# Performance work log

Measured on AMD Instinct MI355X. Metric: run time of the kernel, lower is better.

## Reference

```python
import jax, jax.numpy as jnp
import numpy as np

N = 8192      # total factor-graph rows (detection nodes + association nodes)
ND = N // 2   # detection-node rows; rest are association (edge) rows
D_RAW = 74    # raw input dim; last 10 cols = convex hull (5 points x 2 coords)
EPS = 1e-5    # BatchNorm eps


def _adjs():
    # signed factor-graph adjacencies with self-loops marking row type
    rng = np.random.RandomState(0)
    deg = 8
    node_adj = np.zeros((N, N), np.float32)
    edge_adj = np.zeros((N, N), np.float32)
    nbr = rng.randint(ND, N, size=(ND, deg))
    node_adj[np.repeat(np.arange(ND), deg), nbr.ravel()] = rng.choice([-1.0, 1.0], ND * deg).astype(np.float32)
    node_adj[np.arange(ND), np.arange(ND)] = 1.0
    nbr2 = rng.randint(0, ND, size=(N - ND, deg))
    edge_adj[np.repeat(np.arange(ND, N), deg), nbr2.ravel()] = rng.choice([-1.0, 1.0], (N - ND) * deg).astype(np.float32)
    edge_adj[np.arange(ND, N), np.arange(ND, N)] = 1.0
    return jnp.asarray(node_adj), jnp.asarray(edge_adj)


def setup_inputs() -> dict:
    key = jax.random.key(0)
    ks = jax.random.split(key, 16)
    node_adj, edge_adj = _adjs()

    def lin(k, fi, fo):
        return jax.random.normal(k, (fi, fo), jnp.float32) / np.sqrt(fi)

    inp = {"x": jax.random.normal(ks[0], (N, D_RAW), jnp.float32),
           "node_adj": node_adj, "edge_adj": edge_adj}
    # PointNetfeatsmall: 1x1 conv stack 3->16->32->64 with eval-mode BatchNorm
    for i, (fi, fo) in enumerate([(3, 16), (16, 32), (32, 64)], 1):
        k = jax.random.split(ks[i], 5)
        inp[f"pn_w{i}"] = lin(k[0], fi, fo)
        inp[f"pn_b{i}"] = 0.1 * jax.random.normal(k[1], (fo,), jnp.float32)
        inp[f"pn_g{i}"] = 1.0 + 0.1 * jax.random.normal(k[2], (fo,), jnp.float32)
        inp[f"pn_be{i}"] = 0.1 * jax.random.normal(k[3], (fo,), jnp.float32)
        inp[f"pn_m{i}"] = 0.1 * jax.random.normal(k[4], (fo,), jnp.float32)
        inp[f"pn_v{i}"] = jnp.ones((fo,), jnp.float32)
    # FactorGraphConvolution weights (msg_type='concat' -> in dim doubles)
    for i, (fi, fo) in enumerate([(256, 64), (128, 64), (128, 1)], 1):
        k = jax.random.split(ks[10 + i], 2)
        inp[f"gc{i}_wn"] = lin(k[0], fi, fo)
        inp[f"gc{i}_we"] = lin(k[1], fi, fo)
        inp[f"gc{i}_bn"] = jnp.zeros((fo,), jnp.float32)
        inp[f"gc{i}_be"] = jnp.zeros((fo,), jnp.float32)
    inp["gc3_bn"] = jnp.full((1,), -4.595, jnp.float32)  # nn.init.constant_ in TrackMPNN.__init__
    inp["gc3_be"] = jnp.full((1,), 4.595, jnp.float32)
    return inp


def _bn(h, g, b, m, v):  # h: [N, C, P], eval-mode BatchNorm1d
    return (h - m[:, None]) * (g[:, None] / jnp.sqrt(v[:, None] + EPS)) + b[:, None]


def _fgc(h, node_adj, edge_adj, wn, we, bn_, be_, relu):
    # concat(self, aggregated-neighbors) -> linear; node/edge rows use their own branch
    node_out = jnp.concatenate([h, node_adj @ h], axis=1) @ wn + bn_
    edge_out = jnp.concatenate([h, edge_adj @ h], axis=1) @ we + be_
    out = jnp.where((jnp.diag(node_adj) != 0)[:, None], node_out, edge_out)
    return jax.nn.relu(out) if relu else out


def reference(x, node_adj, edge_adj,
              pn_w1, pn_b1, pn_g1, pn_be1, pn_m1, pn_v1,
              pn_w2, pn_b2, pn_g2, pn_be2, pn_m2, pn_v2,
              pn_w3, pn_b3, pn_g3, pn_be3, pn_m3, pn_v3,
              gc1_wn, gc1_we, gc1_bn, gc1_be,
              gc2_wn, gc2_we, gc2_bn, gc2_be,
              gc3_wn, gc3_we, gc3_bn, gc3_be):
    # convex hull branch: [N, 3, 5] (third coordinate zero-padded)
    ch = jnp.concatenate([x[:, -10:].reshape(-1, 2, 5),
                          jnp.zeros((x.shape[0], 1, 5), x.dtype)], axis=1)
    h = jax.nn.relu(_bn(jnp.einsum('ncp,cd->ndp', ch, pn_w1) + pn_b1[:, None], pn_g1, pn_be1, pn_m1, pn_v1))
    h = jax.nn.relu(_bn(jnp.einsum('ncp,cd->ndp', h, pn_w2) + pn_b2[:, None], pn_g2, pn_be2, pn_m2, pn_v2))
    h = _bn(jnp.einsum('ncp,cd->ndp', h, pn_w3) + pn_b3[:, None], pn_g3, pn_be3, pn_m3, pn_v3)
    feat = h.max(axis=2)                       # PointNet global max pool -> [N, 64]
    h = jnp.concatenate([x[:, :-10], feat], axis=1)  # [N, 128]
    h = _fgc(h, node_adj, edge_adj, gc1_wn, gc1_we, gc1_bn, gc1_be, True)
    h = _fgc(h, node_adj, edge_adj, gc2_wn, gc2_we, gc2_bn, gc2_be, True)
    h = _fgc(h, node_adj, edge_adj, gc3_wn, gc3_we, gc3_bn, gc3_be, False)
    return jax.nn.sigmoid(h)                   # [N, 1]
```

## Files before the change

kernel.cpp:

```cpp
#include <hip/hip_runtime.h>
#include <math.h>

#define NROWS 8192
#define NDET  4096

static constexpr int OFF_SGN = 65536;
static constexpr int OFF_PN  = 131072;
static constexpr int OFF_H1  = 1703936;
static constexpr int OFF_H2  = 2228224;

__global__ __launch_bounds__(256) void k_front(
    const float* __restrict__ nodeA, const float* __restrict__ edgeA,
    int* __restrict__ idx, float* __restrict__ sgn,
    const float* __restrict__ x,
    const float* __restrict__ w1, const float* __restrict__ b1,
    const float* __restrict__ g1, const float* __restrict__ be1,
    const float* __restrict__ m1, const float* __restrict__ v1,
    const float* __restrict__ w2, const float* __restrict__ b2,
    const float* __restrict__ g2, const float* __restrict__ be2,
    const float* __restrict__ m2, const float* __restrict__ v2,
    const float* __restrict__ w3, const float* __restrict__ b3,
    const float* __restrict__ g3, const float* __restrict__ be3,
    const float* __restrict__ m3, const float* __restrict__ v3,
    float* __restrict__ pn)
{
    __shared__ int   scnt;
    __shared__ float fw[2720];
    int t = threadIdx.x;

    if (blockIdx.x >= 512) {
        int row = blockIdx.x - 512;
        const float* src; int col0;
        if (row < NDET) { src = nodeA + (size_t)row * NROWS + NDET; col0 = NDET; }
        else            { src = edgeA + (size_t)row * NROWS;        col0 = 0;    }
        if (t == 0) scnt = 0;
        __syncthreads();
        const float4* s4 = (const float4*)src;
        #pragma unroll
        for (int it = 0; it < 4; ++it) {
            float4 v = s4[t + it * 256];
            int cb = col0 + (t + it * 256) * 4;
            if (v.x != 0.f) { int p = atomicAdd(&scnt, 1); idx[row * 8 + p] = cb;     sgn[row * 8 + p] = v.x; }
            if (v.y != 0.f) { int p = atomicAdd(&scnt, 1); idx[row * 8 + p] = cb + 1; sgn[row * 8 + p] = v.y; }
            if (v.z != 0.f) { int p = atomicAdd(&scnt, 1); idx[row * 8 + p] = cb + 2; sgn[row * 8 + p] = v.z; }
            if (v.w != 0.f) { int p = atomicAdd(&scnt, 1); idx[row * 8 + p] = cb + 3; sgn[row * 8 + p] = v.w; }
        }
        __syncthreads();
        for (int p = scnt + t; p < 8; p += 256) { idx[row * 8 + p] = 0; sgn[row * 8 + p] = 0.f; }
        return;
    }

    for (int i = t; i < 48; i += 256)  { int d = i & 15; fw[i]       = w1[i] * g1[d] * rsqrtf(v1[d] + 1e-5f); }
    for (int i = t; i < 16; i += 256)  {                 fw[48 + i]  = (b1[i] - m1[i]) * g1[i] * rsqrtf(v1[i] + 1e-5f) + be1[i]; }
    for (int i = t; i < 512; i += 256) { int d = i & 31; fw[64 + i]  = w2[i] * g2[d] * rsqrtf(v2[d] + 1e-5f); }
    for (int i = t; i < 32; i += 256)  {                 fw[576 + i] = (b2[i] - m2[i]) * g2[i] * rsqrtf(v2[i] + 1e-5f) + be2[i]; }
    for (int i = t; i < 2048; i += 256){ int d = i & 63; fw[608 + i] = w3[i] * g3[d] * rsqrtf(v3[d] + 1e-5f); }
    for (int i = t; i < 64; i += 256)  {                 fw[2656 + i]= (b3[i] - m3[i]) * g3[i] * rsqrtf(v3[i] + 1e-5f) + be3[i]; }
    __syncthreads();

    int lane = t & 63;
    int wv   = t >> 6;
    int l15  = lane & 15, l31 = lane & 31;
    int rowbase = (blockIdx.x * 4 + wv) * 4;

    for (int r = rowbase; r < rowbase + 4; ++r) {
        float val  = (lane < 10) ? x[(size_t)r * 74 + 64 + lane] : 0.f;
        float vmax = -3.0e38f;
        #pragma unroll
        for (int p = 0; p < 5; ++p) {
            float a0 = __shfl(val, p, 64);
            float a1 = __shfl(val, p + 5, 64);
            float h1v = fmaxf(0.f, a0 * fw[l15] + a1 * fw[16 + l15] + fw[48 + l15]);
            float s2 = fw[576 + l31];
            #pragma unroll
            for (int d = 0; d < 16; ++d)
                s2 += __shfl(h1v, d, 64) * fw[64 + d * 32 + l31];
            float h2v = fmaxf(0.f, s2);
            float s3 = fw[2656 + lane];
            #pragma unroll
            for (int e = 0; e < 32; ++e)
                s3 += __shfl(h2v, e, 64) * fw[608 + e * 64 + lane];
            vmax = fmaxf(vmax, s3);
        }
        pn[(size_t)r * 64 + lane] = vmax;
    }
}

__global__ __launch_bounds__(256) void k_fgc1(
    const float* __restrict__ x, const float* __restrict__ pn,
    const int* __restrict__ idx, const float* __restrict__ sgn,
    const float* __restrict__ wn, const float* __restrict__ we,
    const float* __restrict__ bn, const float* __restrict__ be,
    float* __restrict__ out)
{
    __shared__ float inb[16 * 260];
    __shared__ int   lidx[128];
    __shared__ float lsgn[128];
    int t = threadIdx.x;
    int r0 = blockIdx.x * 16;
    if (t < 128) {
        int ir = t >> 3, j = t & 7;
        lidx[t] = idx[(r0 + ir) * 8 + j];
        lsgn[t] = sgn[(r0 + ir) * 8 + j];
    }
    __syncthreads();

    int f   = t & 127;
    int rrb = t >> 7;
    #pragma unroll
    for (int pass = 0; pass < 8; ++pass) {
        int rr = rrb + pass * 2;
        int r  = r0 + rr;
        float own = (f < 64) ? x[(size_t)r * 74 + f] : pn[(size_t)r * 64 + (f - 64)];
        float acc = own;
        #pragma unroll
        for (int j = 0; j < 8; ++j) {
            int nb   = lidx[rr * 8 + j];
            float sg = lsgn[rr * 8 + j];
            float v  = (f < 64) ? x[(size_t)nb * 74 + f] : pn[(size_t)nb * 64 + (f - 64)];
            acc += sg * v;
        }
        inb[rr * 260 + f]       = own;
        inb[rr * 260 + 128 + f] = acc;
    }
    __syncthreads();

    int r_l = t >> 4, cg = t & 15, c0 = cg * 4;
    bool isnode = (blockIdx.x < 256);
    const float* W = isnode ? wn : we;
    const float* B = isnode ? bn : be;
    float a0 = B[c0], a1 = B[c0 + 1], a2 = B[c0 + 2], a3 = B[c0 + 3];
    #pragma unroll
    for (int kg = 0; kg < 64; ++kg) {
        float4 a = *(const float4*)&inb[r_l * 260 + kg * 4];
        const float* av = &a.x;
        #pragma unroll
        for (int kk = 0; kk < 4; ++kk) {
            float4 w = *(const float4*)&W[(kg * 4 + kk) * 64 + c0];
            a0 += av[kk] * w.x; a1 += av[kk] * w.y;
            a2 += av[kk] * w.z; a3 += av[kk] * w.w;
        }
    }
    float4 o;
    o.x = fmaxf(a0, 0.f); o.y = fmaxf(a1, 0.f);
    o.z = fmaxf(a2, 0.f); o.w = fmaxf(a3, 0.f);
    *(float4*)&out[(size_t)(r0 + r_l) * 64 + c0] = o;
}

__global__ __launch_bounds__(256) void k_fgc2(
    const float* __restrict__ h, const int* __restrict__ idx,
    const float* __restrict__ sgn,
    const float* __restrict__ wn, const float* __restrict__ we,
    const float* __restrict__ bn, const float* __restrict__ be,
    float* __restrict__ out)
{
    __shared__ float inb[16 * 132];
    __shared__ int   lidx[128];
    __shared__ float lsgn[128];
    int t = threadIdx.x;
    int r0 = blockIdx.x * 16;
    if (t < 128) {
        int ir = t >> 3, j = t & 7;
        lidx[t] = idx[(r0 + ir) * 8 + j];
        lsgn[t] = sgn[(r0 + ir) * 8 + j];
    }
    __syncthreads();

    int f   = t & 63;
    int rrb = t >> 6;
    #pragma unroll
    for (int pass = 0; pass < 4; ++pass) {
        int rr = rrb + pass * 4;
        int r  = r0 + rr;
        float own = h[(size_t)r * 64 + f];
        float acc = own;
        #pragma unroll
        for (int j = 0; j < 8; ++j) {
            int nb   = lidx[rr * 8 + j];
            float sg = lsgn[rr * 8 + j];
            acc += sg * h[(size_t)nb * 64 + f];
        }
        inb[rr * 132 + f]      = own;
        inb[rr * 132 + 64 + f] = acc;
    }
    __syncthreads();

    int r_l = t >> 4, cg = t & 15, c0 = cg * 4;
    bool isnode = (blockIdx.x < 256);
    const float* W = isnode ? wn : we;
    const float* B = isnode ? bn : be;
    float a0 = B[c0], a1 = B[c0 + 1], a2 = B[c0 + 2], a3 = B[c0 + 3];
    #pragma unroll
    for (int kg = 0; kg < 32; ++kg) {
        float4 a = *(const float4*)&inb[r_l * 132 + kg * 4];
        const float* av = &a.x;
        #pragma unroll
        for (int kk = 0; kk < 4; ++kk) {
            float4 w = *(const float4*)&W[(kg * 4 + kk) * 64 + c0];
            a0 += av[kk] * w.x; a1 += av[kk] * w.y;
            a2 += av[kk] * w.z; a3 += av[kk] * w.w;
        }
    }
    float4 o;
    o.x = fmaxf(a0, 0.f); o.y = fmaxf(a1, 0.f);
    o.z = fmaxf(a2, 0.f); o.w = fmaxf(a3, 0.f);
    *(float4*)&out[(size_t)(r0 + r_l) * 64 + c0] = o;
}

__global__ __launch_bounds__(256) void k_gc3(
    const float* __restrict__ h2, const int* __restrict__ idx,
    const float* __restrict__ sgn,
    const float* __restrict__ wn, const float* __restrict__ we,
    const float* __restrict__ bn, const float* __restrict__ be,
    float* __restrict__ out)
{
    int lane = threadIdx.x & 63;
    int row  = blockIdx.x * 4 + (threadIdx.x >> 6);
    float own = h2[(size_t)row * 64 + lane];
    float agg = own;
    #pragma unroll
    for (int j = 0; j < 8; ++j) {
        int nb   = idx[row * 8 + j];
        float sg = sgn[row * 8 + j];
        agg += sg * h2[(size_t)nb * 64 + lane];
    }
    bool isnode = row < NDET;
    const float* w = isnode ? wn : we;
    float bias = isnode ? bn[0] : be[0];
    float acc = own * w[lane] + agg * w[64 + lane];
    #pragma unroll
    for (int off = 32; off > 0; off >>= 1)
        acc += __shfl_xor(acc, off, 64);
    if (lane == 0)
        out[row] = 1.f / (1.f + expf(-(acc + bias)));
}

extern "C" void kernel_launch(void* const* d_in, const int* in_sizes, int n_in,
                              void* d_out, int out_size, void* d_ws, size_t ws_size,
                              hipStream_t stream)
{
    const float* x     = (const float*)d_in[0];
    const float* nodeA = (const float*)d_in[1];
    const float* edgeA = (const float*)d_in[2];
    const float* pw1 = (const float*)d_in[3];  const float* pb1 = (const float*)d_in[4];
    const float* pg1 = (const float*)d_in[5];  const float* pe1 = (const float*)d_in[6];
    const float* pm1 = (const float*)d_in[7];  const float* pv1 = (const float*)d_in[8];
    const float* pw2 = (const float*)d_in[9];  const float* pb2 = (const float*)d_in[10];
    const float* pg2 = (const float*)d_in[11]; const float* pe2 = (const float*)d_in[12];
    const float* pm2 = (const float*)d_in[13]; const float* pv2 = (const float*)d_in[14];
    const float* pw3 = (const float*)d_in[15]; const float* pb3 = (const float*)d_in[16];
    const float* pg3 = (const float*)d_in[17]; const float* pe3 = (const float*)d_in[18];
    const float* pm3 = (const float*)d_in[19]; const float* pv3 = (const float*)d_in[20];
    const float* g1wn = (const float*)d_in[21]; const float* g1we = (const float*)d_in[22];
    const float* g1bn = (const float*)d_in[23]; const float* g1be = (const float*)d_in[24];
    const float* g2wn = (const float*)d_in[25]; const float* g2we = (const float*)d_in[26];
    const float* g2bn = (const float*)d_in[27]; const float* g2be = (const float*)d_in[28];
    const float* g3wn = (const float*)d_in[29]; const float* g3we = (const float*)d_in[30];
    const float* g3bn = (const float*)d_in[31]; const float* g3be = (const float*)d_in[32];

    float* ws  = (float*)d_ws;
    int*   idx = (int*)ws;
    float* sgn = ws + OFF_SGN;
    float* pn  = ws + OFF_PN;
    float* h1  = ws + OFF_H1;
    float* h2  = ws + OFF_H2;
    float* out = (float*)d_out;

    k_front<<<512 + NROWS, 256, 0, stream>>>(nodeA, edgeA, idx, sgn, x,
        pw1, pb1, pg1, pe1, pm1, pv1,
        pw2, pb2, pg2, pe2, pm2, pv2,
        pw3, pb3, pg3, pe3, pm3, pv3, pn);
    k_fgc1<<<512, 256, 0, stream>>>(x, pn, idx, sgn, g1wn, g1we, g1bn, g1be, h1);
    k_fgc2<<<512, 256, 0, stream>>>(h1, idx, sgn, g2wn, g2we, g2bn, g2be, h2);
    k_gc3<<<2048, 256, 0, stream>>>(h2, idx, sgn, g3wn, g3we, g3bn, g3be, out);
}
```

Before: 522.8 us.

## Fuse three graph-conv layers into one persistent kernel with grid barriers

Merges the three graph-convolution kernels into a single 512-block kernel separated by software grid-wide barriers built on atomic counters, which k_front resets each call. This removes two kernel launches and their gaps, and lets each block keep its neighbour index and sign lists in shared memory across layers. In exchange it depends on all 512 blocks being co-resident to avoid deadlock, and adds spin-wait barrier cost.

```diff
diff --git a/kernel.cpp b/kernel.cpp
--- a/kernel.cpp
+++ b/kernel.cpp
@@ -8,6 +8,9 @@
 static constexpr int OFF_PN  = 131072;
 static constexpr int OFF_H1  = 1703936;
 static constexpr int OFF_H2  = 2228224;
+static constexpr int OFF_BAR = 2752512;
+
+#define TAIL_BLOCKS 512
 
 __global__ __launch_bounds__(256) void k_front(
     const float* __restrict__ nodeA, const float* __restrict__ edgeA,
@@ -22,7 +25,7 @@
     const float* __restrict__ w3, const float* __restrict__ b3,
     const float* __restrict__ g3, const float* __restrict__ be3,
     const float* __restrict__ m3, const float* __restrict__ v3,
-    float* __restrict__ pn)
+    float* __restrict__ pn, int* __restrict__ bar)
 {
     __shared__ int   scnt;
     __shared__ float fw[2720];
@@ -50,6 +53,8 @@
         return;
     }
 
+    if (blockIdx.x == 0 && t < 2) bar[t] = 0;
+
     for (int i = t; i < 48; i += 256)  { int d = i & 15; fw[i]       = w1[i] * g1[d] * rsqrtf(v1[d] + 1e-5f); }
     for (int i = t; i < 16; i += 256)  {                 fw[48 + i]  = (b1[i] - m1[i]) * g1[i] * rsqrtf(v1[i] + 1e-5f) + be1[i]; }
     for (int i = t; i < 512; i += 256) { int d = i & 31; fw[64 + i]  = w2[i] * g2[d] * rsqrtf(v2[d] + 1e-5f); }
@@ -86,18 +91,38 @@
     }
 }
 
-__global__ __launch_bounds__(256) void k_fgc1(
+__device__ __forceinline__ void gridbar(int* cnt)
+{
+    __syncthreads();
+    if (threadIdx.x == 0) {
+        __threadfence();
+        __hip_atomic_fetch_add(cnt, 1, __ATOMIC_RELEASE, __HIP_MEMORY_SCOPE_AGENT);
+        while (__hip_atomic_load(cnt, __ATOMIC_ACQUIRE, __HIP_MEMORY_SCOPE_AGENT) < TAIL_BLOCKS)
+            __builtin_amdgcn_s_sleep(2);
+    }
+    __syncthreads();
+    __threadfence();
+}
+
+__global__ __launch_bounds__(256, 2) void k_tail(
     const float* __restrict__ x, const float* __restrict__ pn,
     const int* __restrict__ idx, const float* __restrict__ sgn,
-    const float* __restrict__ wn, const float* __restrict__ we,
-    const float* __restrict__ bn, const float* __restrict__ be,
-    float* __restrict__ out)
+    const float* __restrict__ g1wn, const float* __restrict__ g1we,
+    const float* __restrict__ g1bn, const float* __restrict__ g1be,
+    const float* __restrict__ g2wn, const float* __restrict__ g2we,
+    const float* __restrict__ g2bn, const float* __restrict__ g2be,
+    const float* __restrict__ g3wn, const float* __restrict__ g3we,
+    const float* __restrict__ g3bn, const float* __restrict__ g3be,
+    float* __restrict__ h1, float* __restrict__ h2, float* __restrict__ out,
+    int* bar)
 {
     __shared__ float inb[16 * 260];
     __shared__ int   lidx[128];
     __shared__ float lsgn[128];
     int t = threadIdx.x;
     int r0 = blockIdx.x * 16;
+    bool isnode = (blockIdx.x < 256);
+
     if (t < 128) {
         int ir = t >> 3, j = t & 7;
         lidx[t] = idx[(r0 + ir) * 8 + j];
@@ -105,134 +130,110 @@
     }
     __syncthreads();
 
-    int f   = t & 127;
-    int rrb = t >> 7;
-    #pragma unroll
-    for (int pass = 0; pass < 8; ++pass) {
-        int rr = rrb + pass * 2;
-        int r  = r0 + rr;
-        float own = (f < 64) ? x[(size_t)r * 74 + f] : pn[(size_t)r * 64 + (f - 64)];
-        float acc = own;
-        #pragma unroll
-        for (int j = 0; j < 8; ++j) {
-            int nb   = lidx[rr * 8 + j];
-            float sg = lsgn[rr * 8 + j];
-            float v  = (f < 64) ? x[(size_t)nb * 74 + f] : pn[(size_t)nb * 64 + (f - 64)];
-            acc += sg * v;
-        }
-        inb[rr * 260 + f]       = own;
-        inb[rr * 260 + 128 + f] = acc;
-    }
-    __syncthreads();
-
-    int r_l = t >> 4, cg = t & 15, c0 = cg * 4;
-    bool isnode = (blockIdx.x < 256);
-    const float* W = isnode ? wn : we;
-    const float* B = isnode ? bn : be;
-    float a0 = B[c0], a1 = B[c0 + 1], a2 = B[c0 + 2], a3 = B[c0 + 3];
-    #pragma unroll
-    for (int kg = 0; kg < 64; ++kg) {
-        float4 a = *(const float4*)&inb[r_l * 260 + kg * 4];
-        const float* av = &a.x;
-        #pragma unroll
-        for (int kk = 0; kk < 4; ++kk) {
-            float4 w = *(const float4*)&W[(kg * 4 + kk) * 64 + c0];
-            a0 += av[kk] * w.x; a1 += av[kk] * w.y;
-            a2 += av[kk] * w.z; a3 += av[kk] * w.w;
-        }
-    }
-    float4 o;
-    o.x = fmaxf(a0, 0.f); o.y = fmaxf(a1, 0.f);
-    o.z = fmaxf(a2, 0.f); o.w = fmaxf(a3, 0.f);
-    *(float4*)&out[(size_t)(r0 + r_l) * 64 + c0] = o;
-}
-
-__global__ __launch_bounds__(256) void k_fgc2(
-    const float* __restrict__ h, const int* __restrict__ idx,
-    const float* __restrict__ sgn,
-    const float* __restrict__ wn, const float* __restrict__ we,
-    const float* __restrict__ bn, const float* __restrict__ be,
-    float* __restrict__ out)
-{
-    __shared__ float inb[16 * 132];
-    __shared__ int   lidx[128];
-    __shared__ float lsgn[128];
-    int t = threadIdx.x;
-    int r0 = blockIdx.x * 16;
-    if (t < 128) {
-        int ir = t >> 3, j = t & 7;
-        lidx[t] = idx[(r0 + ir) * 8 + j];
-        lsgn[t] = sgn[(r0 + ir) * 8 + j];
-    }
-    __syncthreads();
-
-    int f   = t & 63;
-    int rrb = t >> 6;
-    #pragma unroll
-    for (int pass = 0; pass < 4; ++pass) {
-        int rr = rrb + pass * 4;
-        int r  = r0 + rr;
-        float own = h[(size_t)r * 64 + f];
-        float acc = own;
-        #pragma unroll
-        for (int j = 0; j < 8; ++j) {
-            int nb   = lidx[rr * 8 + j];
-            float sg = lsgn[rr * 8 + j];
-            acc += sg * h[(size_t)nb * 64 + f];
-        }
-        inb[rr * 132 + f]      = own;
-        inb[rr * 132 + 64 + f] = acc;
-    }
-    __syncthreads();
-
-    int r_l = t >> 4, cg = t & 15, c0 = cg * 4;
-    bool isnode = (blockIdx.x < 256);
-    const float* W = isnode ? wn : we;
-    const float* B = isnode ? bn : be;
-    float a0 = B[c0], a1 = B[c0 + 1], a2 = B[c0 + 2], a3 = B[c0 + 3];
-    #pragma unroll
-    for (int kg = 0; kg < 32; ++kg) {
-        float4 a = *(const float4*)&inb[r_l * 132 + kg * 4];
-        const float* av = &a.x;
-        #pragma unroll
-        for (int kk = 0; kk < 4; ++kk) {
-            float4 w = *(const float4*)&W[(kg * 4 + kk) * 64 + c0];
-            a0 += av[kk] * w.x; a1 += av[kk] * w.y;
-            a2 += av[kk] * w.z; a3 += av[kk] * w.w;
-        }
-    }
-    float4 o;
-    o.x = fmaxf(a0, 0.f); o.y = fmaxf(a1, 0.f);
-    o.z = fmaxf(a2, 0.f); o.w = fmaxf(a3, 0.f);
-    *(float4*)&out[(size_t)(r0 + r_l) * 64 + c0] = o;
-}
-
-__global__ __launch_bounds__(256) void k_gc3(
-    const float* __restrict__ h2, const int* __restrict__ idx,
-    const float* __restrict__ sgn,
-    const float* __restrict__ wn, const float* __restrict__ we,
-    const float* __restrict__ bn, const float* __restrict__ be,
-    float* __restrict__ out)
-{
-    int lane = threadIdx.x & 63;
-    int row  = blockIdx.x * 4 + (threadIdx.x >> 6);
-    float own = h2[(size_t)row * 64 + lane];
-    float agg = own;
-    #pragma unroll
-    for (int j = 0; j < 8; ++j) {
-        int nb   = idx[row * 8 + j];
-        float sg = sgn[row * 8 + j];
-        agg += sg * h2[(size_t)nb * 64 + lane];
-    }
-    bool isnode = row < NDET;
-    const float* w = isnode ? wn : we;
-    float bias = isnode ? bn[0] : be[0];
-    float acc = own * w[lane] + agg * w[64 + lane];
-    #pragma unroll
-    for (int off = 32; off > 0; off >>= 1)
-        acc += __shfl_xor(acc, off, 64);
-    if (lane == 0)
-        out[row] = 1.f / (1.f + expf(-(acc + bias)));
+    {
+        int f = t & 127, rrb = t >> 7;
+        #pragma unroll
+        for (int pass = 0; pass < 8; ++pass) {
+            int rr = rrb + pass * 2;
+            int r  = r0 + rr;
+            float own = (f < 64) ? x[(size_t)r * 74 + f] : pn[(size_t)r * 64 + (f - 64)];
+            float acc = own;
+            #pragma unroll
+            for (int j = 0; j < 8; ++j) {
+                int nb   = lidx[rr * 8 + j];
+                float sg = lsgn[rr * 8 + j];
+                float v  = (f < 64) ? x[(size_t)nb * 74 + f] : pn[(size_t)nb * 64 + (f - 64)];
+                acc += sg * v;
+            }
+            inb[rr * 260 + f]       = own;
+            inb[rr * 260 + 128 + f] = acc;
+        }
+        __syncthreads();
+        int r_l = t >> 4, c0 = (t & 15) * 4;
+        const float* W = isnode ? g1wn : g1we;
+        const float* B = isnode ? g1bn : g1be;
+        float a0 = B[c0], a1 = B[c0 + 1], a2 = B[c0 + 2], a3 = B[c0 + 3];
+        #pragma unroll
+        for (int kg = 0; kg < 64; ++kg) {
+            float4 a = *(const float4*)&inb[r_l * 260 + kg * 4];
+            const float* av = &a.x;
+            #pragma unroll
+            for (int kk = 0; kk < 4; ++kk) {
+                float4 w = *(const float4*)&W[(kg * 4 + kk) * 64 + c0];
+                a0 += av[kk] * w.x; a1 += av[kk] * w.y;
+                a2 += av[kk] * w.z; a3 += av[kk] * w.w;
+            }
+        }
+        float4 o;
+        o.x = fmaxf(a0, 0.f); o.y = fmaxf(a1, 0.f);
+        o.z = fmaxf(a2, 0.f); o.w = fmaxf(a3, 0.f);
+        *(float4*)&h1[(size_t)(r0 + r_l) * 64 + c0] = o;
+    }
+    gridbar(&bar[0]);
+    __syncthreads();
+
+    {
+        int f = t & 63, rrb = t >> 6;
+        #pragma unroll
+        for (int pass = 0; pass < 4; ++pass) {
+            int rr = rrb + pass * 4;
+            int r  = r0 + rr;
+            float own = h1[(size_t)r * 64 + f];
+            float acc = own;
+            #pragma unroll
+            for (int j = 0; j < 8; ++j) {
+                int nb   = lidx[rr * 8 + j];
+                float sg = lsgn[rr * 8 + j];
+                acc += sg * h1[(size_t)nb * 64 + f];
+            }
+            inb[rr * 132 + f]      = own;
+            inb[rr * 132 + 64 + f] = acc;
+        }
+        __syncthreads();
+        int r_l = t >> 4, c0 = (t & 15) * 4;
+        const float* W = isnode ? g2wn : g2we;
+        const float* B = isnode ? g2bn : g2be;
+        float a0 = B[c0], a1 = B[c0 + 1], a2 = B[c0 + 2], a3 = B[c0 + 3];
+        #pragma unroll
+        for (int kg = 0; kg < 32; ++kg) {
+            float4 a = *(const float4*)&inb[r_l * 132 + kg * 4];
+            const float* av = &a.x;
+            #pragma unroll
+            for (int kk = 0; kk < 4; ++kk) {
+                float4 w = *(const float4*)&W[(kg * 4 + kk) * 64 + c0];
+                a0 += av[kk] * w.x; a1 += av[kk] * w.y;
+                a2 += av[kk] * w.z; a3 += av[kk] * w.w;
+            }
+        }
+        float4 o;
+        o.x = fmaxf(a0, 0.f); o.y = fmaxf(a1, 0.f);
+        o.z = fmaxf(a2, 0.f); o.w = fmaxf(a3, 0.f);
+        *(float4*)&h2[(size_t)(r0 + r_l) * 64 + c0] = o;
+    }
+    gridbar(&bar[1]);
+
+    {
+        int lane = t & 63, wv = t >> 6;
+        const float* w = isnode ? g3wn : g3we;
+        float bias = isnode ? g3bn[0] : g3be[0];
+        for (int rr = wv * 4; rr < wv * 4 + 4; ++rr) {
+            int row = r0 + rr;
+            float own = h2[(size_t)row * 64 + lane];
+            float agg = own;
+            #pragma unroll
+            for (int j = 0; j < 8; ++j) {
+                int nb   = lidx[rr * 8 + j];
+                float sg = lsgn[rr * 8 + j];
+                agg += sg * h2[(size_t)nb * 64 + lane];
+            }
+            float acc = own * w[lane] + agg * w[64 + lane];
+            #pragma unroll
+            for (int off = 32; off > 0; off >>= 1)
+                acc += __shfl_xor(acc, off, 64);
+            if (lane == 0)
+                out[row] = 1.f / (1.f + expf(-(acc + bias)));
+        }
+    }
 }
 
 extern "C" void kernel_launch(void* const* d_in, const int* in_sizes, int n_in,
@@ -264,13 +265,17 @@
     float* pn  = ws + OFF_PN;
     float* h1  = ws + OFF_H1;
     float* h2  = ws + OFF_H2;
+    int*   bar = (int*)(ws + OFF_BAR);
     float* out = (float*)d_out;
 
     k_front<<<512 + NROWS, 256, 0, stream>>>(nodeA, edgeA, idx, sgn, x,
         pw1, pb1, pg1, pe1, pm1, pv1,
         pw2, pb2, pg2, pe2, pm2, pv2,
-        pw3, pb3, pg3, pe3, pm3, pv3, pn);
-    k_fgc1<<<512, 256, 0, stream>>>(x, pn, idx, sgn, g1wn, g1we, g1bn, g1be, h1);
-    k_fgc2<<<512, 256, 0, stream>>>(h1, idx, sgn, g2wn, g2we, g2bn, g2be, h2);
-    k_gc3<<<2048, 256, 0, stream>>>(h2, idx, sgn, g3wn, g3we, g3bn, g3be, out);
-}
+        pw3, pb3, pg3, pe3, pm3, pv3, pn, bar);
+
+    k_tail<<<TAIL_BLOCKS, 256, 0, stream>>>(x, pn, idx, sgn,
+        g1wn, g1we, g1bn, g1be,
+        g2wn, g2we, g2bn, g2be,
+        g3wn, g3we, g3bn, g3be,
+        h1, h2, out, bar);
+}
```

Result: slower. 714.1 us (+36.6%).
